# Performance work log

Hardware: AMD Instinct MI355X
Metric: run time of the kernel (lower is better)

## Reference

```python
import jax, jax.numpy as jnp
import numpy as np

B, H, T, D = 2, 16, 2048, 64


def setup_inputs() -> dict:
    key = jax.random.key(0)
    kq, kk, kv, km = jax.random.split(key, 4)
    q = jax.random.normal(kq, (B, H, T, D), dtype=jnp.float32)
    k = jax.random.normal(kk, (B, H, T, D), dtype=jnp.float32)
    v = jax.random.normal(kv, (B, H, T, D), dtype=jnp.float32)
    # boolean mask, True = masked out (broadcast over batch and heads)
    mask = jax.random.randint(km, (1, 1, T, T), 0, 2).astype(jnp.bool_)
    return {"q": q, "k": k, "v": v, "mask": mask}


def reference(q, k, v, mask):
    scale = q.shape[-1] ** (-0.5)
    # [B,H,T,T] score matrix (materialized, as in the original)
    scores = jnp.einsum("bhqd,bhkd->bhqk", q, k) * scale
    scores = jnp.where(mask, jnp.float32(-10000.0), scores)
    attn = jax.nn.softmax(scores, axis=-1)
    attn = jnp.where(mask, jnp.float32(0.0), attn)
    return jnp.einsum("bhqk,bhkd->bhqd", attn, v)
```

## Files before the change

kernel.cpp:

```cpp
#include <hip/hip_runtime.h>
#include <hip/hip_bf16.h>

typedef __bf16 bf16x8 __attribute__((ext_vector_type(8)));
typedef __bf16 bf16x4 __attribute__((ext_vector_type(4)));
typedef float  f32x4  __attribute__((ext_vector_type(4)));

#define T_SEQ 2048
#define D_HEAD 64
#define BH_N 32
#define NT_TILES (T_SEQ / 64)
#define QT_N 8
#define IMG_BYTES 16384
#define SCALE_LOG2 0.18033688011112042f

#define WS_IMG ((size_t)0)
#define WS_MB  ((size_t)16u << 20)

static __device__ __forceinline__ f32x4 mfma32(bf16x8 a, bf16x8 b, f32x4 c) {
    return __builtin_amdgcn_mfma_f32_16x16x32_bf16(a, b, c, 0, 0, 0);
}

static __device__ __forceinline__ float fast_exp2(float x) {
#if __has_builtin(__builtin_amdgcn_exp2f)
    return __builtin_amdgcn_exp2f(x);
#else
    return exp2f(x);
#endif
}

static __device__ __forceinline__ int sext_bit(unsigned w, int idx) {
#if __has_builtin(__builtin_amdgcn_sbfe)
    return __builtin_amdgcn_sbfe((int)w, idx, 1);
#else
    return (int)(w << (31 - idx)) >> 31;
#endif
}

static __device__ __forceinline__ void gload16(const void* g, void* l, int lane) {
#if __has_builtin(__builtin_amdgcn_global_load_lds)
    (void)lane;
    __builtin_amdgcn_global_load_lds(
        (const __attribute__((address_space(1))) void*)g,
        (__attribute__((address_space(3))) void*)l, 16, 0, 0);
#else
    *((f32x4*)l + lane) = *(const f32x4*)g;
#endif
}


__global__ __launch_bounds__(256) void prep_kv(const float* __restrict__ k,
                                               const float* __restrict__ v,
                                               char* __restrict__ img) {
    __shared__ __bf16 t[64][72];
    const int bh = blockIdx.y, tt = blockIdx.x, tid = threadIdx.x;
    char* ob = img + ((size_t)bh * NT_TILES + tt) * IMG_BYTES;
    {
        const int kr = tid >> 2, qd = tid & 3, ke = kr & 7;
        const size_t base = ((size_t)bh * T_SEQ + tt * 64 + kr) * D_HEAD + qd * 16;
        const float4 a0 = *(const float4*)(k + base);
        const float4 a1 = *(const float4*)(k + base + 4);
        const float4 a2 = *(const float4*)(k + base + 8);
        const float4 a3 = *(const float4*)(k + base + 12);
        bf16x8 w0, w1;
        w0[0]=(__bf16)a0.x; w0[1]=(__bf16)a0.y; w0[2]=(__bf16)a0.z; w0[3]=(__bf16)a0.w;
        w0[4]=(__bf16)a1.x; w0[5]=(__bf16)a1.y; w0[6]=(__bf16)a1.z; w0[7]=(__bf16)a1.w;
        w1[0]=(__bf16)a2.x; w1[1]=(__bf16)a2.y; w1[2]=(__bf16)a2.z; w1[3]=(__bf16)a2.w;
        w1[4]=(__bf16)a3.x; w1[5]=(__bf16)a3.y; w1[6]=(__bf16)a3.z; w1[7]=(__bf16)a3.w;
        *(bf16x8*)(ob + kr * 128 + (((2 * qd + 0) ^ ke) << 4)) = w0;
        *(bf16x8*)(ob + kr * 128 + (((2 * qd + 1) ^ ke) << 4)) = w1;
    }
    {
        const int tr = tid >> 4, c4 = (tid & 15) * 4;
        const float* src = v + ((size_t)bh * T_SEQ + tt * 64) * D_HEAD;
#pragma unroll
        for (int p = 0; p < 4; ++p) {
            const int row = p * 16 + tr;
            const float4 f = *(const float4*)(src + row * D_HEAD + c4);
            t[c4+0][row] = (__bf16)f.x; t[c4+1][row] = (__bf16)f.y;
            t[c4+2][row] = (__bf16)f.z; t[c4+3][row] = (__bf16)f.w;
        }
        __syncthreads();
        const int d = tid >> 2;
        char* vb = ob + 8192 + d * 128;
#pragma unroll
        for (int mi = 0; mi < 2; ++mi) {
            const int m  = (tid & 3) * 2 + mi;
            const int u  = m ^ (d & 7);
            const int k0 = (u & 1) * 32 + (u >> 1) * 4;
            const bf16x4 lo = *(const bf16x4*)&t[d][k0];
            const bf16x4 hi = *(const bf16x4*)&t[d][k0 + 16];
            *(bf16x8*)(vb + m * 16) = __builtin_shufflevector(lo, hi, 0,1,2,3,4,5,6,7);
        }
    }
}

__global__ void mpack(const int* __restrict__ m, unsigned* __restrict__ nbt) {
    const int i = blockIdx.x * 256 + threadIdx.x;
    const unsigned long long b = __ballot(m[i] != 0);
    if ((threadIdx.x & 63) == 0) {
        const int wi  = i >> 6;
        const int row = wi >> 5;
        const int t   = wi & 31;
        nbt[(size_t)(t * 2 + 0) * 2048 + row] = ~(unsigned)b;
        nbt[(size_t)(t * 2 + 1) * 2048 + row] = ~(unsigned)(b >> 32);
    }
}


__global__ __launch_bounds__(512, 2) void attn18(
    const float* __restrict__ q, const char* __restrict__ img,
    const unsigned* __restrict__ nbt, float* __restrict__ out)
{
    const int l   = blockIdx.x;
    const int bh  = ((l & 7) << 2) | ((l >> 3) & 3);
    const int qt  = l >> 5;

    const int tid = threadIdx.x, wave = tid >> 6, lane = tid & 63;
    const int g = lane >> 4, ln = lane & 15;
    const int qp = wave & 3, kh = wave >> 2;
    const int g4 = g * 4;

    __shared__ __align__(16) char smem[133120];
    float* Ep = (float*)smem;
    float* Os = (float*)(smem + 131072);

    const int qw = qt * 256 + qp * 64;

    bf16x8 qf[4][2];
#pragma unroll
    for (int qs = 0; qs < 4; ++qs) {
        const float* qpt = q + ((size_t)bh * T_SEQ + qw + qs * 16 + ln) * D_HEAD + g * 8;
#pragma unroll
        for (int kc = 0; kc < 2; ++kc) {
            const float4 f0 = *(const float4*)(qpt + kc * 32);
            const float4 f1 = *(const float4*)(qpt + kc * 32 + 4);
            qf[qs][kc][0]=(__bf16)(f0.x*SCALE_LOG2); qf[qs][kc][1]=(__bf16)(f0.y*SCALE_LOG2);
            qf[qs][kc][2]=(__bf16)(f0.z*SCALE_LOG2); qf[qs][kc][3]=(__bf16)(f0.w*SCALE_LOG2);
            qf[qs][kc][4]=(__bf16)(f1.x*SCALE_LOG2); qf[qs][kc][5]=(__bf16)(f1.y*SCALE_LOG2);
            qf[qs][kc][6]=(__bf16)(f1.z*SCALE_LOG2); qf[qs][kc][7]=(__bf16)(f1.w*SCALE_LOG2);
        }
    }

    f32x4 o[4][4];
#pragma unroll
    for (int qs = 0; qs < 4; ++qs)
#pragma unroll
        for (int mt = 0; mt < 4; ++mt) o[qs][mt] = (f32x4){0.f, 0.f, 0.f, 0.f};
    f32x4 osum[4] = { (f32x4){0.f,0.f,0.f,0.f}, (f32x4){0.f,0.f,0.f,0.f},
                      (f32x4){0.f,0.f,0.f,0.f}, (f32x4){0.f,0.f,0.f,0.f} };
    const bf16x8 ones8 = { (__bf16)1.0f, (__bf16)1.0f, (__bf16)1.0f, (__bf16)1.0f,
                           (__bf16)1.0f, (__bf16)1.0f, (__bf16)1.0f, (__bf16)1.0f };
    const f32x4 z4 = (f32x4){0.f, 0.f, 0.f, 0.f};

    const char* ibase = img + (size_t)bh * (NT_TILES * (size_t)IMG_BYTES);
    const unsigned* nb_base = nbt + (size_t)kh * 2048 + qw;

    int koffs[2][2];
#pragma unroll
    for (int ntl = 0; ntl < 2; ++ntl) {
        const int row = (2 * kh + ntl) * 16 + ln;
        const int rb = row * 128 + ((g ^ (ln & 7)) << 4);
        koffs[ntl][0] = rb; koffs[ntl][1] = rb ^ 64;
    }
    int voffs[4];
#pragma unroll
    for (int mt = 0; mt < 4; ++mt)
        voffs[mt] = (mt * 16 + ln) * 128 + ((((g << 1) | kh) ^ (ln & 7)) << 4);

    char* const b0 = smem;              char* const b1 = smem + 16384;
    char* const b2 = smem + 32768;      char* const b3 = smem + 49152;
    char* const b4 = smem + 65536;      char* const b5 = smem + 81920;
    char* const b6 = smem + 98304;      char* const b7 = smem + 114688;

    auto stage = [&](int tile, char* dstbase) {
        const char* src = ibase + (size_t)tile * IMG_BYTES + wave * 2048 + lane * 16;
        char* dst = dstbase + wave * 2048;
        gload16(src, dst, lane);
        gload16(src + 1024, dst + 1024, lane);
    };

    auto compute_tile = [&](const char* KB, const unsigned* nw) {
        const char* VB = KB + 8192;
        unsigned nbs[4];
#pragma unroll
        for (int qs = 0; qs < 4; ++qs) nbs[qs] = nw[qs] >> g4;

        bf16x8 ka[2][2];
#pragma unroll
        for (int ntl = 0; ntl < 2; ++ntl) {
            ka[ntl][0] = *(const bf16x8*)(KB + koffs[ntl][0]);
            ka[ntl][1] = *(const bf16x8*)(KB + koffs[ntl][1]);
        }

        bf16x8 pa8[4];
#pragma unroll
        for (int ntl = 0; ntl < 2; ++ntl) {
            f32x4 c[4];
            __builtin_amdgcn_s_setprio(1);
#pragma unroll
            for (int qs = 0; qs < 4; ++qs) {
                c[qs] = mfma32(ka[ntl][0], qf[qs][0], z4);
                c[qs] = mfma32(ka[ntl][1], qf[qs][1], c[qs]);
            }
            __builtin_amdgcn_s_setprio(0);
#pragma unroll
            for (int qs = 0; qs < 4; ++qs) {
#pragma unroll
                for (int r = 0; r < 4; ++r) {
                    const float e = fast_exp2(c[qs][r]);
                    const int keep = sext_bit(nbs[qs], ntl * 16 + r);
                    const float p = __builtin_bit_cast(float,
                        __builtin_bit_cast(unsigned, e) & (unsigned)keep);
                    pa8[qs][ntl * 4 + r] = (__bf16)p;
                }
            }
        }

        bf16x8 vv[4];
#pragma unroll
        for (int mt = 0; mt < 4; ++mt) vv[mt] = *(const bf16x8*)(VB + voffs[mt]);
        __builtin_amdgcn_s_setprio(1);
#pragma unroll
        for (int qs = 0; qs < 4; ++qs) osum[qs] = mfma32(pa8[qs], ones8, osum[qs]);
#pragma unroll
        for (int mt = 0; mt < 4; ++mt)
#pragma unroll
            for (int qs = 0; qs < 4; ++qs)
                o[qs][mt] = mfma32(pa8[qs], vv[mt], o[qs][mt]);
        __builtin_amdgcn_s_setprio(0);
    };

    auto window = [&](const char* X, const char* Y, int t, char* SX, char* SY) {
        if (t + 6 < NT_TILES) { stage(t + 6, SX); stage(t + 7, SY); }
        const unsigned* p0 = nb_base + (size_t)t * 4096;
        const unsigned* p1 = p0 + 4096;
        unsigned nw0[4], nw1[4];
#pragma unroll
        for (int qs = 0; qs < 4; ++qs) { nw0[qs] = p0[qs * 16 + ln]; nw1[qs] = p1[qs * 16 + ln]; }
        compute_tile(X, nw0);
        compute_tile(Y, nw1);
        __syncthreads();
    };

    stage(0, b0); stage(1, b1); stage(2, b2);
    stage(3, b3); stage(4, b4); stage(5, b5);
    __syncthreads();

#pragma unroll 1
    for (int i = 0; i < 4; ++i) {
        const int t = 8 * i;
        window(b0, b1, t,     b6, b7);
        window(b2, b3, t + 2, b0, b1);
        window(b4, b5, t + 4, b2, b3);
        window(b6, b7, t + 6, b4, b5);
    }

#pragma unroll
    for (int pass = 0; pass < 2; ++pass) {
        if ((qp >> 1) == pass) {
            const int qpl = qp & 1;
#pragma unroll
            for (int qs = 0; qs < 4; ++qs) {
#pragma unroll
                for (int mt = 0; mt < 4; ++mt)
#pragma unroll
                    for (int r = 0; r < 4; ++r)
                        Ep[(size_t)kh * 8192 + (qpl * 64 + qs * 16 + g * 4 + r) * 64 + mt * 16 + ln] = o[qs][mt][r];
                if (ln == 0) {
#pragma unroll
                    for (int r = 0; r < 4; ++r)
                        Os[kh * 128 + qpl * 64 + qs * 16 + g * 4 + r] = osum[qs][r];
                }
            }
        }
        __syncthreads();
#pragma unroll
        for (int p2 = 0; p2 < 4; ++p2) {
            const int idx = p2 * 512 + tid;
            const int row = idx >> 4, c4 = (idx & 15) * 4;
            const float sl = Os[row] + Os[128 + row];
            const float inv = (sl > 0.f) ? (1.f / sl) : 0.f;
            const float4 a  = *(const float4*)(Ep + row * 64 + c4);
            const float4 b4v = *(const float4*)(Ep + 8192 + row * 64 + c4);
            const float4 st = { (a.x + b4v.x) * inv, (a.y + b4v.y) * inv,
                                (a.z + b4v.z) * inv, (a.w + b4v.w) * inv };
            *(float4*)(out + ((size_t)bh * T_SEQ + qt * 256 + pass * 128 + row) * D_HEAD + c4) = st;
        }
        if (pass == 0) __syncthreads();
    }
}

extern "C" void kernel_launch(void* const* d_in, const int* in_sizes, int n_in,
                              void* d_out, int out_size, void* d_ws, size_t ws_size,
                              hipStream_t stream) {
    const float* q    = (const float*)d_in[0];
    const float* k    = (const float*)d_in[1];
    const float* v    = (const float*)d_in[2];
    const int*   mask = (const int*)d_in[3];
    float*       out  = (float*)d_out;

    char* img = (char*)d_ws + WS_IMG;
    unsigned* nbt = (unsigned*)((char*)d_ws + WS_MB);

    prep_kv<<<dim3(NT_TILES, BH_N), 256, 0, stream>>>(k, v, img);
    mpack<<<(T_SEQ * T_SEQ) / 256, 256, 0, stream>>>(mask, nbt);
    attn18<<<dim3(QT_N * BH_N), 512, 0, stream>>>(q, img, nbt, out);
}
```

Before: 163.3 us.

## Shrink attention blocks to 4 waves with double-buffered LDS and more blocks

Halves the query tile per block from 256 to 128 rows, giving 4 waves instead of 8 and twice as many blocks. It also replaces the 8-deep K/V tile ring with simple double buffering, which cuts LDS from about 130KB to 33KB so more blocks fit per CU. The aim is better occupancy and CU coverage, since 256 blocks sat below the number of CUs. The cost is that each K/V tile is loaded by twice as many blocks, and the shallower prefetch leaves less room to hide load latency.

```diff
diff --git a/kernel.cpp b/kernel.cpp
--- a/kernel.cpp
+++ b/kernel.cpp
@@ -9,7 +9,7 @@
 #define D_HEAD 64
 #define BH_N 32
 #define NT_TILES (T_SEQ / 64)
-#define QT_N 8
+#define QT_N 16
 #define IMG_BYTES 16384
 #define SCALE_LOG2 0.18033688011112042f
 
@@ -107,24 +107,25 @@
 }
 
 
-__global__ __launch_bounds__(512, 2) void attn18(
+__global__ __launch_bounds__(256, 4) void attn19(
     const float* __restrict__ q, const char* __restrict__ img,
     const unsigned* __restrict__ nbt, float* __restrict__ out)
 {
     const int l   = blockIdx.x;
-    const int bh  = ((l & 7) << 2) | ((l >> 3) & 3);
-    const int qt  = l >> 5;
+    const int m_  = l >> 3;
+    const int bh  = ((l & 7) << 2) | (m_ & 3);
+    const int qt  = m_ >> 2;
 
     const int tid = threadIdx.x, wave = tid >> 6, lane = tid & 63;
     const int g = lane >> 4, ln = lane & 15;
-    const int qp = wave & 3, kh = wave >> 2;
+    const int qp = wave & 1, kh = wave >> 1;
     const int g4 = g * 4;
 
-    __shared__ __align__(16) char smem[133120];
+    __shared__ __align__(16) char smem[33280];
     float* Ep = (float*)smem;
-    float* Os = (float*)(smem + 131072);
-
-    const int qw = qt * 256 + qp * 64;
+    float* Os = (float*)(smem + 32768);
+
+    const int qw = qt * 128 + qp * 64;
 
     bf16x8 qf[4][2];
 #pragma unroll
@@ -167,16 +168,16 @@
     for (int mt = 0; mt < 4; ++mt)
         voffs[mt] = (mt * 16 + ln) * 128 + ((((g << 1) | kh) ^ (ln & 7)) << 4);
 
-    char* const b0 = smem;              char* const b1 = smem + 16384;
-    char* const b2 = smem + 32768;      char* const b3 = smem + 49152;
-    char* const b4 = smem + 65536;      char* const b5 = smem + 81920;
-    char* const b6 = smem + 98304;      char* const b7 = smem + 114688;
+    char* buf0 = smem;
+    char* buf1 = smem + 16384;
 
     auto stage = [&](int tile, char* dstbase) {
-        const char* src = ibase + (size_t)tile * IMG_BYTES + wave * 2048 + lane * 16;
-        char* dst = dstbase + wave * 2048;
+        const char* src = ibase + (size_t)tile * IMG_BYTES + wave * 4096 + lane * 16;
+        char* dst = dstbase + wave * 4096;
         gload16(src, dst, lane);
         gload16(src + 1024, dst + 1024, lane);
+        gload16(src + 2048, dst + 2048, lane);
+        gload16(src + 3072, dst + 3072, lane);
     };
 
     auto compute_tile = [&](const char* KB, const unsigned* nw) {
@@ -230,61 +231,62 @@
         __builtin_amdgcn_s_setprio(0);
     };
 
-    auto window = [&](const char* X, const char* Y, int t, char* SX, char* SY) {
-        if (t + 6 < NT_TILES) { stage(t + 6, SX); stage(t + 7, SY); }
-        const unsigned* p0 = nb_base + (size_t)t * 4096;
-        const unsigned* p1 = p0 + 4096;
-        unsigned nw0[4], nw1[4];
-#pragma unroll
-        for (int qs = 0; qs < 4; ++qs) { nw0[qs] = p0[qs * 16 + ln]; nw1[qs] = p1[qs * 16 + ln]; }
-        compute_tile(X, nw0);
-        compute_tile(Y, nw1);
+    stage(0, buf0);
+    unsigned mwA[4], mwB[4];
+#pragma unroll
+    for (int qs = 0; qs < 4; ++qs) mwA[qs] = nb_base[qs * 16 + ln];
+    __syncthreads();
+
+#pragma unroll 1
+    for (int i = 0; i < NT_TILES / 2; ++i) {
+        const int t = 2 * i;
+        stage(t + 1, buf1);
+        {
+            const unsigned* p = nb_base + (size_t)(t + 1) * 4096;
+#pragma unroll
+            for (int qs = 0; qs < 4; ++qs) mwB[qs] = p[qs * 16 + ln];
+        }
+        compute_tile(buf0, mwA);
         __syncthreads();
-    };
-
-    stage(0, b0); stage(1, b1); stage(2, b2);
-    stage(3, b3); stage(4, b4); stage(5, b5);
-    __syncthreads();
-
-#pragma unroll 1
-    for (int i = 0; i < 4; ++i) {
-        const int t = 8 * i;
-        window(b0, b1, t,     b6, b7);
-        window(b2, b3, t + 2, b0, b1);
-        window(b4, b5, t + 4, b2, b3);
-        window(b6, b7, t + 6, b4, b5);
+        if (i < NT_TILES / 2 - 1) {
+            stage(t + 2, buf0);
+            const unsigned* p = nb_base + (size_t)(t + 2) * 4096;
+#pragma unroll
+            for (int qs = 0; qs < 4; ++qs) mwA[qs] = p[qs * 16 + ln];
+        }
+        compute_tile(buf1, mwB);
+        __syncthreads();
     }
 
 #pragma unroll
     for (int pass = 0; pass < 2; ++pass) {
-        if ((qp >> 1) == pass) {
-            const int qpl = qp & 1;
+        if (qp == pass) {
 #pragma unroll
             for (int qs = 0; qs < 4; ++qs) {
 #pragma unroll
                 for (int mt = 0; mt < 4; ++mt)
 #pragma unroll
                     for (int r = 0; r < 4; ++r)
-                        Ep[(size_t)kh * 8192 + (qpl * 64 + qs * 16 + g * 4 + r) * 64 + mt * 16 + ln] = o[qs][mt][r];
+                        Ep[(size_t)kh * 4096 + (qs * 16 + g * 4 + r) * 64 + mt * 16 + ln] = o[qs][mt][r];
                 if (ln == 0) {
 #pragma unroll
                     for (int r = 0; r < 4; ++r)
-                        Os[kh * 128 + qpl * 64 + qs * 16 + g * 4 + r] = osum[qs][r];
+                        Os[kh * 64 + qs * 16 + g * 4 + r] = osum[qs][r];
                 }
             }
         }
         __syncthreads();
 #pragma unroll
         for (int p2 = 0; p2 < 4; ++p2) {
-            const int idx = p2 * 512 + tid;
+            const int idx = p2 * 256 + tid;
             const int row = idx >> 4, c4 = (idx & 15) * 4;
-            const float sl = Os[row] + Os[128 + row];
+            const float sl = Os[row] + Os[64 + row];
             const float inv = (sl > 0.f) ? (1.f / sl) : 0.f;
             const float4 a  = *(const float4*)(Ep + row * 64 + c4);
-            const float4 b4v = *(const float4*)(Ep + 8192 + row * 64 + c4);
-            const float4 st = { (a.x + b4v.x) * inv, (a.y + b4v.y) * inv,
-                                (a.z + b4v.z) * inv, (a.w + b4v.w) * inv };
-            *(float4*)(out + ((size_t)bh * T_SEQ + qt * 256 + pass * 128 + row) * D_HEAD + c4) = st;
+            const float4 b4 = *(const float4*)(Ep + 4096 + row * 64 + c4);
+            const float4 st = { (a.x + b4.x) * inv, (a.y + b4.y) * inv,
+                                (a.z + b4.z) * inv, (a.w + b4.w) * inv };
+            *(float4*)(out + ((size_t)bh * T_SEQ + qt * 128 + pass * 64 + row) * D_HEAD + c4) = st;
         }
         if (pass == 0) __syncthreads();
     }
@@ -304,5 +306,5 @@
 
     prep_kv<<<dim3(NT_TILES, BH_N), 256, 0, stream>>>(k, v, img);
     mpack<<<(T_SEQ * T_SEQ) / 256, 256, 0, stream>>>(mask, nbt);
-    attn18<<<dim3(QT_N * BH_N), 512, 0, stream>>>(q, img, nbt, out);
-}
+    attn19<<<dim3(QT_N * BH_N), 256, 0, stream>>>(q, img, nbt, out);
+}
```

Result: slower. 345.3 us (+111.5%).
